# Performance work log

Hardware: AMD Instinct MI355X
Metric: run time of the kernel (lower is better)

## Reference

```python
import jax, jax.numpy as jnp
import numpy as np
from jax.scipy.special import logsumexp


def setup_inputs() -> dict:
    key = jax.random.key(0)
    k = jax.random.split(key, 8)
    B, T, K, L = 32, 128, 16, 16
    s = 0.05
    y_batch = jax.random.uniform(k[0], (B, T, 1, 28, 28), dtype=jnp.float32)
    enc_w1 = jax.random.normal(k[1], (400, 784), dtype=jnp.float32) * s
    enc_b1 = jnp.zeros((400,), jnp.float32)
    enc_w2 = jax.random.normal(k[2], (2 * L, 400), dtype=jnp.float32) * s
    enc_b2 = jnp.zeros((2 * L,), jnp.float32)
    dec_fc_w = jax.random.normal(k[3], (400, L + K), dtype=jnp.float32) * s
    dec_fc_b = jnp.zeros((400,), jnp.float32)
    dec_w = jax.random.normal(k[4], (784, 400), dtype=jnp.float32) * s
    dec_b = jnp.zeros((784,), jnp.float32)
    log_pi = jnp.zeros((K,), jnp.float32)
    log_A = jax.random.normal(k[5], (K, K), dtype=jnp.float32)
    log_A = log_A.at[jnp.arange(K), jnp.arange(K)].set(-1e9)  # fill_diagonal_(-1e9)
    eps = jax.random.normal(k[6], (B * T, L), dtype=jnp.float32)
    return dict(y_batch=y_batch, enc_w1=enc_w1, enc_b1=enc_b1, enc_w2=enc_w2,
                enc_b2=enc_b2, dec_fc_w=dec_fc_w, dec_fc_b=dec_fc_b, dec_w=dec_w,
                dec_b=dec_b, log_pi=log_pi, log_A=log_A, eps=eps)


def reference(y_batch, enc_w1, enc_b1, enc_w2, enc_b2, dec_fc_w, dec_fc_b,
              dec_w, dec_b, log_pi, log_A, eps):
    B, T = y_batch.shape[0], y_batch.shape[1]
    K = log_pi.shape[0]
    L = eps.shape[1]
    N = B * T
    # ---- VAE emission log-likelihoods (compute_log_bk); dropout in eval mode ----
    y_flat = y_batch.reshape(N, 784)
    h = jax.nn.relu(y_flat @ enc_w1.T + enc_b1)                 # [N,400]
    ml = h @ enc_w2.T + enc_b2                                   # [N,2L]
    mu, logvar = ml[:, :L], ml[:, L:]
    z = mu + eps * jnp.exp(0.5 * logvar)                         # reparameterize
    # decode(z, one_hot(k)) for all k at once: split cat-linear into z part + k column
    Wz, Wx = dec_fc_w[:, :L], dec_fc_w[:, L:]                    # [400,L],[400,K]
    base = z @ Wz.T + dec_fc_b                                   # [N,400]
    hk = jax.nn.relu(base[None, :, :] + Wx.T[:, None, :])        # [K,N,400]
    y_rec = jax.nn.sigmoid(jnp.einsum('knh,oh->kno', hk, dec_w) + dec_b)  # [K,N,784]
    # binary_cross_entropy with torch's log clamp at -100
    logp = jnp.clip(jnp.log(y_rec), -100.0, None)
    log1mp = jnp.clip(jnp.log(1.0 - y_rec), -100.0, None)
    bce = -(y_flat[None] * logp + (1.0 - y_flat[None]) * log1mp)  # [K,N,784]
    recon = bce.sum(-1) / 100.0                                   # [K,N]
    log_bk = (-recon).reshape(K, B, T).transpose(1, 2, 0)         # [B,T,K]
    # ---- forward-backward in log domain ----
    lp = jnp.log(jax.nn.softmax(log_pi) + 1e-9)
    lA = jnp.log(jax.nn.softmax(log_A, axis=1) + 1e-9)
    lb_rest = jnp.moveaxis(log_bk[:, 1:], 1, 0)                   # [T-1,B,K]
    a0 = lp + log_bk[:, 0]                                        # [B,K]

    def fstep(prev, lb_t):
        cur = logsumexp(prev[:, :, None] + lA[None], axis=1) + lb_t
        return cur, cur

    _, alphas = jax.lax.scan(fstep, a0, lb_rest)
    log_alpha = jnp.concatenate([a0[:, None], jnp.moveaxis(alphas, 0, 1)], axis=1)  # [B,T,K]

    bT = jnp.zeros((B, K), log_bk.dtype)

    def bstep(nxt, lb_t1):
        cur = logsumexp(lA[None] + (lb_t1 + nxt)[:, None, :], axis=2)
        return cur, cur

    _, betas = jax.lax.scan(bstep, bT, lb_rest, reverse=True)     # betas[t] = beta_t, t=0..T-2
    log_beta = jnp.concatenate([jnp.moveaxis(betas, 0, 1), bT[:, None]], axis=1)  # [B,T,K]

    lg = log_alpha + log_beta
    log_gamma = lg - logsumexp(lg, axis=2, keepdims=True)

    lxi = (log_alpha[:, :-1, :, None] + lA[None, None]
           + (log_bk[:, 1:] + log_beta[:, 1:])[:, :, None, :])    # [B,T-1,K,K]
    lxi = lxi - logsumexp(lxi, axis=(2, 3), keepdims=True)
    return jnp.exp(log_gamma), jnp.exp(lxi)
```

## Files before the change

kernel.cpp:

```cpp
#include <hip/hip_runtime.h>
#include <math.h>


typedef _Float16 h8v __attribute__((ext_vector_type(8)));
typedef _Float16 h4v __attribute__((ext_vector_type(4)));
typedef float f16v __attribute__((ext_vector_type(16)));

__device__ __forceinline__ void gll16(const void* g, void* l) {
  __builtin_amdgcn_global_load_lds(
      (const __attribute__((address_space(1))) void*)g,
      (__attribute__((address_space(3))) void*)l, 16, 0, 0);
}

__global__ __launch_bounds__(256)
void k_prep(const float* __restrict__ dw, const float* __restrict__ ew1,
            _Float16* __restrict__ dwh, _Float16* __restrict__ w1h,
            float* __restrict__ lb) {
  int idx = blockIdx.x * 256 + threadIdx.x;
  if (idx < 65536) lb[idx] = 0.f;
  if (idx < 896 * 448) {
    int o = idx / 448, h2 = idx - o * 448;
    float v = (o < 784 && h2 < 400) ? dw[o * 400 + h2] : 0.f;
    dwh[idx] = (_Float16)v;
  } else if (idx < 896 * 448 + 512 * 800) {
    int j = idx - 896 * 448;
    int i = j / 800, kc = j - i * 800;
    float v = (i < 400 && kc < 784) ? ew1[i * 784 + kc] : 0.f;
    w1h[j] = (_Float16)v;
  }
}

#define E1ST 40
__global__ __launch_bounds__(256, 2)
void k_enc1(const float* __restrict__ y, const _Float16* __restrict__ w1h,
            const float* __restrict__ b1, float* __restrict__ hout) {
  __shared__ __align__(16) _Float16 Ah[64 * E1ST];
  __shared__ __align__(16) _Float16 Bh[128 * E1ST];
  const int tid = threadIdx.x;
  const int i0 = blockIdx.x * 128;
  const int n0 = blockIdx.y * 64;
  const int wav = tid >> 6, lane = tid & 63;
  const int wn = wav >> 1, wi = wav & 1;
  const int ln = lane & 31, kg = lane >> 5;

  f16v acc[2];
#pragma unroll
  for (int j = 0; j < 2; ++j)
#pragma unroll
    for (int r = 0; r < 16; ++r) acc[j][r] = 0.f;

  const int ar = tid >> 3, ac4 = (tid & 7) * 4;
  const int br = tid >> 2, bg = (tid & 3) * 8;

#pragma unroll 1
  for (int hc = 0; hc < 25; ++hc) {
    const int h0 = hc * 32;
    __syncthreads();
#pragma unroll
    for (int it = 0; it < 2; ++it) {
      int r = ar + 32 * it;
      float4 a = make_float4(0.f, 0.f, 0.f, 0.f);
      if (h0 + ac4 < 784) a = *(const float4*)&y[(n0 + r) * 784 + h0 + ac4];
      h4v hv;
      hv[0] = (_Float16)a.x; hv[1] = (_Float16)a.y;
      hv[2] = (_Float16)a.z; hv[3] = (_Float16)a.w;
      *(h4v*)&Ah[r * E1ST + ac4] = hv;
    }
#pragma unroll
    for (int it = 0; it < 2; ++it) {
      int r = br + 64 * it;
      *(h8v*)&Bh[r * E1ST + bg] = *(const h8v*)&w1h[(i0 + r) * 800 + h0 + bg];
    }
    __syncthreads();
#pragma unroll
    for (int kk = 0; kk < 2; ++kk) {
      const int ko = kk * 16 + kg * 8;
      h8v a  = *(const h8v*)&Ah[(wn * 32 + ln) * E1ST + ko];
      h8v b0 = *(const h8v*)&Bh[(wi * 64 + ln) * E1ST + ko];
      h8v b1 = *(const h8v*)&Bh[(wi * 64 + 32 + ln) * E1ST + ko];
      acc[0] = __builtin_amdgcn_mfma_f32_32x32x16_f16(a, b0, acc[0], 0, 0, 0);
      acc[1] = __builtin_amdgcn_mfma_f32_32x32x16_f16(a, b1, acc[1], 0, 0, 0);
    }
  }
#pragma unroll
  for (int j = 0; j < 2; ++j) {
    const int i = i0 + wi * 64 + j * 32 + ln;
    if (i < 400) {
      const float bias = b1[i];
#pragma unroll
      for (int reg = 0; reg < 16; ++reg) {
        const int row = n0 + wn * 32 + (reg & 3) + 8 * (reg >> 2) + 4 * kg;
        hout[row * 400 + i] = fmaxf(acc[j][reg] + bias, 0.f);
      }
    }
  }
}

__global__ __launch_bounds__(128, 2)
void k_enc2z(const float* __restrict__ h, const float* __restrict__ w2,
             const float* __restrict__ b2, const float* __restrict__ eps,
             float* __restrict__ z) {
  __shared__ __align__(16) float h_lds[16 * 400];
  __shared__ __align__(16) float w2_lds[32 * 404];
  __shared__ float ml_lds[16 * 32];
  const int tid = threadIdx.x;
  const int n0 = blockIdx.x * 16;
  for (int idx = tid; idx < 1600; idx += 128) {
    int r = idx / 100, c = idx - r * 100;
    *(float4*)&h_lds[r * 400 + c * 4] = *(const float4*)&h[(n0 + r) * 400 + c * 4];
  }
  for (int idx = tid; idx < 3200; idx += 128) {
    int r = idx / 100, c = idx - r * 100;
    *(float4*)&w2_lds[r * 404 + c * 4] = *(const float4*)&w2[r * 400 + c * 4];
  }
  __syncthreads();
  const int c_ = tid & 31, n4 = tid >> 5;
  float a0 = 0.f, a1 = 0.f, a2 = 0.f, a3 = 0.f;
  for (int q = 0; q < 100; ++q) {
    float4 wv = *(const float4*)&w2_lds[c_ * 404 + q * 4];
    float4 h0 = *(const float4*)&h_lds[(n4 * 4 + 0) * 400 + q * 4];
    float4 h1 = *(const float4*)&h_lds[(n4 * 4 + 1) * 400 + q * 4];
    float4 h2 = *(const float4*)&h_lds[(n4 * 4 + 2) * 400 + q * 4];
    float4 h3 = *(const float4*)&h_lds[(n4 * 4 + 3) * 400 + q * 4];
    a0 += h0.x * wv.x + h0.y * wv.y + h0.z * wv.z + h0.w * wv.w;
    a1 += h1.x * wv.x + h1.y * wv.y + h1.z * wv.z + h1.w * wv.w;
    a2 += h2.x * wv.x + h2.y * wv.y + h2.z * wv.z + h2.w * wv.w;
    a3 += h3.x * wv.x + h3.y * wv.y + h3.z * wv.z + h3.w * wv.w;
  }
  const float bb = b2[c_];
  ml_lds[(n4 * 4 + 0) * 32 + c_] = a0 + bb;
  ml_lds[(n4 * 4 + 1) * 32 + c_] = a1 + bb;
  ml_lds[(n4 * 4 + 2) * 32 + c_] = a2 + bb;
  ml_lds[(n4 * 4 + 3) * 32 + c_] = a3 + bb;
  __syncthreads();
  for (int t = tid; t < 256; t += 128) {
    int n2 = t >> 4, l = t & 15;
    float mu = ml_lds[n2 * 32 + l];
    float lv = ml_lds[n2 * 32 + 16 + l];
    z[(n0 + n2) * 16 + l] = mu + eps[(n0 + n2) * 16 + l] * expf(0.5f * lv);
  }
}

__global__ __launch_bounds__(256, 2)
void k_basehk(const float* __restrict__ z, const float* __restrict__ dfw,
              const float* __restrict__ dfb, _Float16* __restrict__ hkh) {
  __shared__ float z_lds[16 * 16];
  __shared__ __align__(16) float wz[400 * 20];
  __shared__ __align__(16) float base[16 * 448];
  const int tid = threadIdx.x;
  const int n0 = blockIdx.x * 16;
  if (tid < 64) {
    int n = tid >> 2, c = (tid & 3) * 4;
    *(float4*)&z_lds[n * 16 + c] = *(const float4*)&z[(n0 + n) * 16 + c];
  }
  for (int idx = tid; idx < 1600; idx += 256) {
    int i = idx >> 2, c = (idx & 3) * 4;
    *(float4*)&wz[i * 20 + c] = *(const float4*)&dfw[i * 32 + c];
  }
  __syncthreads();
  for (int idx = tid; idx < 7168; idx += 256) {
    int n = idx / 448, i = idx - n * 448;
    float acc = 0.f;
    if (i < 400) {
      acc = dfb[i];
#pragma unroll
      for (int q = 0; q < 4; ++q) {
        float4 zv = *(const float4*)&z_lds[n * 16 + q * 4];
        float4 wv = *(const float4*)&wz[i * 20 + q * 4];
        acc += zv.x * wv.x + zv.y * wv.y + zv.z * wv.z + zv.w * wv.w;
      }
    }
    base[n * 448 + i] = acc;
  }
  __syncthreads();
  for (int idx = tid; idx < 7168; idx += 256) {
    int k = idx / 448, hh = idx - k * 448;
    wz[idx] = (hh < 400) ? dfw[hh * 32 + 16 + k] : 0.f;
  }
  __syncthreads();
  for (int s = tid; s < 14336; s += 256) {
    int k = s / 896, r2 = s - k * 896;
    int r = r2 / 56, c8 = r2 - r * 56;
    const float* bp = &base[r * 448 + c8 * 8];
    const float* wp = &wz[k * 448 + c8 * 8];
    float4 b0 = *(const float4*)bp, b1 = *(const float4*)(bp + 4);
    float4 w0 = *(const float4*)wp, w1 = *(const float4*)(wp + 4);
    h8v o;
    o[0] = (_Float16)fmaxf(b0.x + w0.x, 0.f);
    o[1] = (_Float16)fmaxf(b0.y + w0.y, 0.f);
    o[2] = (_Float16)fmaxf(b0.z + w0.z, 0.f);
    o[3] = (_Float16)fmaxf(b0.w + w0.w, 0.f);
    o[4] = (_Float16)fmaxf(b1.x + w1.x, 0.f);
    o[5] = (_Float16)fmaxf(b1.y + w1.y, 0.f);
    o[6] = (_Float16)fmaxf(b1.z + w1.z, 0.f);
    o[7] = (_Float16)fmaxf(b1.w + w1.w, 0.f);
    *(h8v*)&hkh[((size_t)k * 4096 + n0 + r) * 448 + c8 * 8] = o;
  }
}

__global__ __launch_bounds__(256, 4)
void k_base(const float* __restrict__ z, const float* __restrict__ dfw,
            const float* __restrict__ dfb, float* __restrict__ basep) {
  __shared__ float z_lds[16 * 16];
  __shared__ __align__(16) float wz_lds[400 * 20];
  const int tid = threadIdx.x;
  const int n0 = blockIdx.x * 16;
  if (tid < 64) {
    int n = tid >> 2, c = (tid & 3) * 4;
    *(float4*)&z_lds[n * 16 + c] = *(const float4*)&z[(n0 + n) * 16 + c];
  }
  for (int idx = tid; idx < 1600; idx += 256) {
    int i = idx >> 2, c = (idx & 3) * 4;
    *(float4*)&wz_lds[i * 20 + c] = *(const float4*)&dfw[i * 32 + c];
  }
  __syncthreads();
  for (int idx = tid; idx < 7168; idx += 256) {
    int n = idx / 448, i = idx - n * 448;
    float acc = 0.f;
    if (i < 400) {
      acc = dfb[i];
#pragma unroll
      for (int q = 0; q < 4; ++q) {
        float4 zv = *(const float4*)&z_lds[n * 16 + q * 4];
        float4 wv = *(const float4*)&wz_lds[i * 20 + q * 4];
        acc += zv.x * wv.x + zv.y * wv.y + zv.z * wv.z + zv.w * wv.w;
      }
    }
    basep[(n0 + n) * 448 + i] = acc;
  }
}

__global__ __launch_bounds__(256, 2)
void k_dec5(const _Float16* __restrict__ hkh, const _Float16* __restrict__ dwh,
            const float* __restrict__ decb, const float* __restrict__ y,
            float* __restrict__ lb) {
  __shared__ __align__(16) _Float16 Ah[2][128 * 64];
  __shared__ __align__(16) _Float16 Bh[2][128 * 64];
  __shared__ float red[256];

  const int tid = threadIdx.x;
  const int id  = blockIdx.x;
  const int lin = (id & 7) * 448 + (id >> 3);
  const int n_i = lin / 112;
  const int rem = lin - n_i * 112;
  const int k   = rem / 7;
  const int ot  = rem - k * 7;
  const int n0  = n_i * 128;
  const int o0  = ot * 128;

  const int wav = tid >> 6, lane = tid & 63;
  const int wn = wav >> 1, wo = wav & 1;
  const int ln = lane & 31, kg = lane >> 5;

  const int l8 = lane >> 3, l7 = lane & 7;
  const int swh = (l7 * 8) ^ (l8 * 8);
  const _Float16* hkk = hkh + (size_t)k * (4096 * 448);
  const _Float16* pA[4];
  const _Float16* pB[4];
#pragma unroll
  for (int i = 0; i < 4; ++i) {
    const int row = wav * 32 + i * 8 + l8;
    pA[i] = hkk + (size_t)(n0 + row) * 448 + swh;
    pB[i] = dwh + (size_t)(o0 + row) * 448 + swh;
  }

  f16v acc[2][2];
#pragma unroll
  for (int i = 0; i < 2; ++i)
#pragma unroll
    for (int j = 0; j < 2; ++j)
#pragma unroll
      for (int r = 0; r < 16; ++r) acc[i][j][r] = 0.f;

#pragma unroll
  for (int i = 0; i < 4; ++i) { gll16(pA[i], &Ah[0][(wav * 4 + i) * 512]); pA[i] += 64; }
#pragma unroll
  for (int i = 0; i < 4; ++i) { gll16(pB[i], &Bh[0][(wav * 4 + i) * 512]); pB[i] += 64; }
  asm volatile("s_waitcnt vmcnt(0)" ::: "memory");
  __builtin_amdgcn_sched_barrier(0);
  __builtin_amdgcn_s_barrier();

  const int e0 = (kg * 8) ^ ((ln & 7) * 8);
  const int arow = (wn * 64 + ln) * 64;
  const int brow = (wo * 64 + ln) * 64;

  int cur = 0;
#pragma unroll 1
  for (int hc = 0; hc < 7; ++hc) {
    if (hc < 6) {
#pragma unroll
      for (int i = 0; i < 4; ++i) { gll16(pA[i], &Ah[cur ^ 1][(wav * 4 + i) * 512]); pA[i] += 64; }
#pragma unroll
      for (int i = 0; i < 4; ++i) { gll16(pB[i], &Bh[cur ^ 1][(wav * 4 + i) * 512]); pB[i] += 64; }
      __builtin_amdgcn_sched_barrier(0);
    }
    const _Float16* Ac = Ah[cur];
    const _Float16* Bc = Bh[cur];
#pragma unroll
    for (int kk = 0; kk < 4; ++kk) {
      const int cx = (kk * 16) ^ e0;
      h8v a0 = *(const h8v*)&Ac[arow + cx];
      h8v a1 = *(const h8v*)&Ac[arow + 2048 + cx];
      h8v b0 = *(const h8v*)&Bc[brow + cx];
      h8v b1 = *(const h8v*)&Bc[brow + 2048 + cx];
      acc[0][0] = __builtin_amdgcn_mfma_f32_32x32x16_f16(a0, b0, acc[0][0], 0, 0, 0);
      acc[1][0] = __builtin_amdgcn_mfma_f32_32x32x16_f16(a1, b0, acc[1][0], 0, 0, 0);
      acc[0][1] = __builtin_amdgcn_mfma_f32_32x32x16_f16(a0, b1, acc[0][1], 0, 0, 0);
      acc[1][1] = __builtin_amdgcn_mfma_f32_32x32x16_f16(a1, b1, acc[1][1], 0, 0, 0);
    }
    if (hc < 6) {
      asm volatile("s_waitcnt vmcnt(0)" ::: "memory");
      __builtin_amdgcn_sched_barrier(0);
      __builtin_amdgcn_s_barrier();
      cur ^= 1;
    }
  }

  const int obase = o0 + wo * 64;
  const float bj0 = (obase + ln < 784) ? decb[obase + ln] : 0.f;
  const float bj1 = (obase + 32 + ln < 784) ? decb[obase + 32 + ln] : 0.f;
#pragma unroll
  for (int i = 0; i < 2; ++i) {
#pragma unroll
    for (int reg = 0; reg < 16; ++reg) {
      const int row = wn * 64 + i * 32 + (reg & 3) + 8 * (reg >> 2) + 4 * kg;
      float v = 0.f;
#pragma unroll
      for (int j = 0; j < 2; ++j) {
        const int o = obase + j * 32 + ln;
        if (o < 784) {
          float x = acc[i][j][reg] + (j ? bj1 : bj0);
          float yv = y[(n0 + row) * 784 + o];
          float spx = fmaxf(x, 0.f) + __logf(1.f + __expf(-fabsf(x)));
          v += spx - yv * x;
        }
      }
      v += __shfl_xor(v, 1, 64);
      v += __shfl_xor(v, 2, 64);
      v += __shfl_xor(v, 4, 64);
      v += __shfl_xor(v, 8, 64);
      v += __shfl_xor(v, 16, 64);
      if (ln == 0) red[wo * 128 + row] = v;
    }
  }
  __syncthreads();
  if (tid < 128) {
    float s = red[tid] + red[128 + tid];
    atomicAdd(&lb[(n0 + tid) * 16 + k], s);
  }
}

#define DST 72
__global__ __launch_bounds__(256, 2)
void k_dec1(const float* __restrict__ basep, const float* __restrict__ dfw,
            const _Float16* __restrict__ dwh, const float* __restrict__ decb,
            const float* __restrict__ y, float* __restrict__ lb) {
  __shared__ __align__(16) _Float16 Ah[128 * DST];
  __shared__ __align__(16) _Float16 Bh[128 * DST];
  __shared__ float wx[448];
  __shared__ float red[256];

  const int tid = threadIdx.x;
  const int id  = blockIdx.x;
  const int lin = (id & 7) * 448 + (id >> 3);
  const int n_i = lin / 112;
  const int rem = lin - n_i * 112;
  const int k   = rem / 7;
  const int ot  = rem - k * 7;
  const int n0  = n_i * 128;
  const int o0  = ot * 128;
  const bool full = (ot < 6);

  const int wav = tid >> 6, lane = tid & 63;
  const int wn = wav >> 1, wo = wav & 1;
  const int ln = lane & 31, kg = lane >> 5;

  for (int i = tid; i < 448; i += 256) wx[i] = (i < 400) ? dfw[i * 32 + 16 + k] : 0.f;

  const int ar = tid >> 4, ac4 = (tid & 15) * 4;
  const int br = tid >> 3, bg = (tid & 7) * 8;
  const float* aptr = basep + (long)(n0 + ar) * 448 + ac4;

  float4 apf[8];
#pragma unroll
  for (int it = 0; it < 8; ++it) apf[it] = *(const float4*)&aptr[(16 * it) * 448];

  f16v acc[2][2];
#pragma unroll
  for (int i = 0; i < 2; ++i)
#pragma unroll
    for (int j = 0; j < 2; ++j)
#pragma unroll
      for (int r = 0; r < 16; ++r) acc[i][j][r] = 0.f;

#pragma unroll 1
  for (int hc = 0; hc < 7; ++hc) {
    const int h0 = hc * 64;
    h8v bpf[4];
#pragma unroll
    for (int it = 0; it < 4; ++it)
      bpf[it] = *(const h8v*)&dwh[(o0 + br + 32 * it) * 448 + h0 + bg];
    __syncthreads();
    {
      float4 w = *(const float4*)&wx[h0 + ac4];
#pragma unroll
      for (int it = 0; it < 8; ++it) {
        int r = ar + 16 * it;
        h4v hv;
        hv[0] = (_Float16)fmaxf(apf[it].x + w.x, 0.f);
        hv[1] = (_Float16)fmaxf(apf[it].y + w.y, 0.f);
        hv[2] = (_Float16)fmaxf(apf[it].z + w.z, 0.f);
        hv[3] = (_Float16)fmaxf(apf[it].w + w.w, 0.f);
        *(h4v*)&Ah[r * DST + ac4] = hv;
      }
    }
#pragma unroll
    for (int it = 0; it < 4; ++it)
      *(h8v*)&Bh[(br + 32 * it) * DST + bg] = bpf[it];
    __syncthreads();
    if (hc < 6) {
      const int hn = (hc + 1) * 64;
#pragma unroll
      for (int it = 0; it < 8; ++it)
        apf[it] = *(const float4*)&aptr[(16 * it) * 448 + hn];
    }
#pragma unroll
    for (int kk = 0; kk < 4; ++kk) {
      const int ko = kk * 16 + kg * 8;
      h8v a0 = *(const h8v*)&Ah[(wn * 64 + ln) * DST + ko];
      h8v a1 = *(const h8v*)&Ah[(wn * 64 + 32 + ln) * DST + ko];
      h8v b0 = *(const h8v*)&Bh[(wo * 64 + ln) * DST + ko];
      h8v b1 = *(const h8v*)&Bh[(wo * 64 + 32 + ln) * DST + ko];
      if (full) {
        acc[0][0] = __builtin_amdgcn_mfma_f32_32x32x16_f16(a0, b0, acc[0][0], 0, 0, 0);
        acc[1][0] = __builtin_amdgcn_mfma_f32_32x32x16_f16(a1, b0, acc[1][0], 0, 0, 0);
        acc[0][1] = __builtin_amdgcn_mfma_f32_32x32x16_f16(a0, b1, acc[0][1], 0, 0, 0);
        acc[1][1] = __builtin_amdgcn_mfma_f32_32x32x16_f16(a1, b1, acc[1][1], 0, 0, 0);
      } else if (wo == 0) {
        acc[0][0] = __builtin_amdgcn_mfma_f32_32x32x16_f16(a0, b0, acc[0][0], 0, 0, 0);
        acc[1][0] = __builtin_amdgcn_mfma_f32_32x32x16_f16(a1, b0, acc[1][0], 0, 0, 0);
      }
    }
  }
  const int obase = o0 + wo * 64;
  const float bj0 = (obase + ln < 784) ? decb[obase + ln] : 0.f;
  const float bj1 = (obase + 32 + ln < 784) ? decb[obase + 32 + ln] : 0.f;
#pragma unroll
  for (int i = 0; i < 2; ++i) {
#pragma unroll
    for (int reg = 0; reg < 16; ++reg) {
      const int row = wn * 64 + i * 32 + (reg & 3) + 8 * (reg >> 2) + 4 * kg;
      float v = 0.f;
#pragma unroll
      for (int j = 0; j < 2; ++j) {
        const int o = obase + j * 32 + ln;
        if (o < 784) {
          float x = acc[i][j][reg] + (j ? bj1 : bj0);
          float yv = y[(n0 + row) * 784 + o];
          float spx = fmaxf(x, 0.f) + __logf(1.f + __expf(-fabsf(x)));
          float t2 = fminf(spx, 100.f);
          float t1 = fminf(spx - x, 100.f);
          v += t2 + yv * (t1 - t2);
        }
      }
      v += __shfl_xor(v, 1, 64);
      v += __shfl_xor(v, 2, 64);
      v += __shfl_xor(v, 4, 64);
      v += __shfl_xor(v, 8, 64);
      v += __shfl_xor(v, 16, 64);
      if (ln == 0) red[wo * 128 + row] = v;
    }
  }
  __syncthreads();
  if (tid < 128) {
    float s = red[tid] + red[128 + tid];
    atomicAdd(&lb[(n0 + tid) * 16 + k], s);
  }
}

__global__ __launch_bounds__(256, 2)
void k_hmm(const float* __restrict__ lb, const float* __restrict__ lpi,
           const float* __restrict__ lA, float* __restrict__ out) {
  __shared__ float btl[128 * 16];
  __shared__ float ah[128 * 16];
  __shared__ float bh[128 * 16];
  __shared__ float braw[128 * 16];
  __shared__ float A_l[16 * 17];
  __shared__ float pi_l[16];
  __shared__ float sinv_l[128];
  const int tid = threadIdx.x;
  const int b = blockIdx.x;

  for (int idx = tid; idx < 512; idx += 256) {
    float4 v = *(const float4*)&lb[b * 2048 + idx * 4];
    v.x *= -0.01f; v.y *= -0.01f; v.z *= -0.01f; v.w *= -0.01f;
    *(float4*)&btl[idx * 4] = v;
  }
  if (tid < 16) {
    const int j = tid;
    float m = -1e30f;
#pragma unroll
    for (int q = 0; q < 16; ++q) m = fmaxf(m, lA[j * 16 + q]);
    float e[16]; float s = 0.f;
#pragma unroll
    for (int q = 0; q < 16; ++q) { e[q] = expf(lA[j * 16 + q] - m); s += e[q]; }
    float inv = 1.f / s;
#pragma unroll
    for (int q = 0; q < 16; ++q) A_l[j * 17 + q] = e[q] * inv + 1e-9f;
  } else if (tid == 16) {
    float m = -1e30f;
#pragma unroll
    for (int q = 0; q < 16; ++q) m = fmaxf(m, lpi[q]);
    float e[16]; float s = 0.f;
#pragma unroll
    for (int q = 0; q < 16; ++q) { e[q] = expf(lpi[q] - m); s += e[q]; }
    float inv = 1.f / s;
#pragma unroll
    for (int q = 0; q < 16; ++q) pi_l[q] = e[q] * inv + 1e-9f;
  }
  __syncthreads();
  if (tid < 128) {
    const int t = tid;
    float v[16]; float m = -1e30f;
#pragma unroll
    for (int q = 0; q < 16; ++q) { v[q] = btl[t * 16 + q]; m = fmaxf(m, v[q]); }
#pragma unroll
    for (int q = 0; q < 16; ++q) btl[t * 16 + q] = expf(v[q] - m);
  }
  __syncthreads();
  const int lane = tid & 63;
  const int kk = lane & 15, grp = lane >> 4;
  if (tid < 64) {
    float v0 = pi_l[kk] * btl[kk];
    float ss0 = v0;
    ss0 += __shfl_xor(ss0, 1, 64); ss0 += __shfl_xor(ss0, 2, 64);
    ss0 += __shfl_xor(ss0, 4, 64); ss0 += __shfl_xor(ss0, 8, 64);
    if (grp == 0) ah[kk] = v0 / ss0;
    for (int t = 1; t < 128; ++t) {
      float acc = 0.f;
#pragma unroll
      for (int jj = 0; jj < 4; ++jj) {
        int j = grp * 4 + jj;
        acc = fmaf(ah[(t - 1) * 16 + j], A_l[j * 17 + kk], acc);
      }
      acc += __shfl_xor(acc, 16, 64);
      acc += __shfl_xor(acc, 32, 64);
      float v = acc * btl[t * 16 + kk];
      float ss = v;
      ss += __shfl_xor(ss, 1, 64); ss += __shfl_xor(ss, 2, 64);
      ss += __shfl_xor(ss, 4, 64); ss += __shfl_xor(ss, 8, 64);
      if (grp == 0) ah[t * 16 + kk] = v / ss;
    }
  } else if (tid < 128) {
    if (grp == 0) bh[127 * 16 + kk] = 1.f;
    for (int t = 126; t >= 0; --t) {
      float acc = 0.f;
#pragma unroll
      for (int q = 0; q < 4; ++q) {
        int k2 = grp * 4 + q;
        acc = fmaf(A_l[kk * 17 + k2], btl[(t + 1) * 16 + k2] * bh[(t + 1) * 16 + k2], acc);
      }
      acc += __shfl_xor(acc, 16, 64);
      acc += __shfl_xor(acc, 32, 64);
      float ss = acc;
      ss += __shfl_xor(ss, 1, 64); ss += __shfl_xor(ss, 2, 64);
      ss += __shfl_xor(ss, 4, 64); ss += __shfl_xor(ss, 8, 64);
      if (grp == 0) { braw[t * 16 + kk] = acc; bh[t * 16 + kk] = acc / ss; }
    }
  }
  __syncthreads();
  if (tid < 128) {
    const int t = tid;
    float g[16]; float s2 = 0.f;
#pragma unroll
    for (int q = 0; q < 16; ++q) { g[q] = ah[t * 16 + q] * bh[t * 16 + q]; s2 += g[q]; }
    float inv = 1.f / s2;
#pragma unroll
    for (int c = 0; c < 4; ++c) {
      float4 o;
      o.x = g[c * 4 + 0] * inv; o.y = g[c * 4 + 1] * inv;
      o.z = g[c * 4 + 2] * inv; o.w = g[c * 4 + 3] * inv;
      *(float4*)&out[(b * 128 + t) * 16 + c * 4] = o;
    }
  } else {
    const int t = tid - 128;
    if (t < 127) {
      float s2 = 0.f;
#pragma unroll
      for (int q = 0; q < 16; ++q) s2 += ah[t * 16 + q] * braw[t * 16 + q];
      sinv_l[t] = 1.f / s2;
    }
  }
  __syncthreads();
  const int j = tid >> 4, k2 = tid & 15;
  const float aj = A_l[j * 17 + k2];
  float* xo = out + 65536 + (size_t)b * 127 * 256 + tid;
  for (int t = 0; t < 127; ++t) {
    float val = ah[t * 16 + j] * aj * btl[(t + 1) * 16 + k2] *
                bh[(t + 1) * 16 + k2] * sinv_l[t];
    xo[t * 256] = val;
  }
}

extern "C" void kernel_launch(void* const* d_in, const int* in_sizes, int n_in,
                              void* d_out, int out_size, void* d_ws, size_t ws_size,
                              hipStream_t stream) {
  (void)in_sizes; (void)n_in; (void)out_size;
  const float* y   = (const float*)d_in[0];
  const float* ew1 = (const float*)d_in[1];
  const float* eb1 = (const float*)d_in[2];
  const float* ew2 = (const float*)d_in[3];
  const float* eb2 = (const float*)d_in[4];
  const float* dfw = (const float*)d_in[5];
  const float* dfb = (const float*)d_in[6];
  const float* dw  = (const float*)d_in[7];
  const float* db  = (const float*)d_in[8];
  const float* lpi = (const float*)d_in[9];
  const float* lA  = (const float*)d_in[10];
  const float* eps = (const float*)d_in[11];
  float* out = (float*)d_out;

  float* ws = (float*)d_ws;
  float* h      = ws;
  float* basep  = ws;
  float* z      = ws + 1835008;
  float* lb     = z + 65536;
  _Float16* dwh = (_Float16*)(lb + 65536);
  _Float16* w1h = dwh + 896 * 448;
  float* gpad   = (float*)(w1h + 512 * 800);
  _Float16* hkh = (_Float16*)(gpad + 65536 * 2 + 4096 + 256);

  const bool big_ws = (ws_size >= 68748288ull);

  k_prep<<<3168, 256, 0, stream>>>(dw, ew1, dwh, w1h, lb);
  k_enc1<<<dim3(4, 64), 256, 0, stream>>>(y, w1h, eb1, h);
  k_enc2z<<<256, 128, 0, stream>>>(h, ew2, eb2, eps, z);
  if (big_ws) {
    k_basehk<<<256, 256, 0, stream>>>(z, dfw, dfb, hkh);
    k_dec5<<<3584, 256, 0, stream>>>(hkh, dwh, db, y, lb);
  } else {
    k_base<<<256, 256, 0, stream>>>(z, dfw, dfb, basep);
    k_dec1<<<3584, 256, 0, stream>>>(basep, dfw, dwh, db, y, lb);
  }
  k_hmm<<<32, 256, 0, stream>>>(lb, lpi, lA, out);
}
```

Before: 375.2 us.

## Pre-convert input images to fp16 and single-buffer decoder GEMM LDS tiles

The prep kernel now also converts the input images to a padded fp16 buffer, stored in the hk workspace region before that region is reused. The encoder GEMM then loads 16-byte fp16 vectors instead of converting fp32 on the fly. The decoder GEMM drops its LDS double buffering and uses a single buffer with two barriers per chunk, which halves LDS use and may raise occupancy but exposes load latency. A separate fp32-input encoder remains for the small-workspace path.

Measured after the change: 325.6 us. 1.15x faster.

```diff
diff --git a/kernel.cpp b/kernel.cpp
--- a/kernel.cpp
+++ b/kernel.cpp
@@ -14,7 +14,8 @@
 
 __global__ __launch_bounds__(256)
 void k_prep(const float* __restrict__ dw, const float* __restrict__ ew1,
-            _Float16* __restrict__ dwh, _Float16* __restrict__ w1h,
+            const float* __restrict__ y, _Float16* __restrict__ dwh,
+            _Float16* __restrict__ w1h, _Float16* __restrict__ yh,
             float* __restrict__ lb) {
   int idx = blockIdx.x * 256 + threadIdx.x;
   if (idx < 65536) lb[idx] = 0.f;
@@ -22,18 +23,79 @@
     int o = idx / 448, h2 = idx - o * 448;
     float v = (o < 784 && h2 < 400) ? dw[o * 400 + h2] : 0.f;
     dwh[idx] = (_Float16)v;
-  } else if (idx < 896 * 448 + 512 * 800) {
+  } else if (idx < 811008) {
     int j = idx - 896 * 448;
     int i = j / 800, kc = j - i * 800;
     float v = (i < 400 && kc < 784) ? ew1[i * 784 + kc] : 0.f;
     w1h[j] = (_Float16)v;
+  } else if (idx < 4087808) {
+    int j = idx - 811008;
+    int n = j / 800, c = j - n * 800;
+    float v = (c < 784) ? y[n * 784 + c] : 0.f;
+    yh[j] = (_Float16)v;
   }
 }
 
 #define E1ST 40
 __global__ __launch_bounds__(256, 2)
-void k_enc1(const float* __restrict__ y, const _Float16* __restrict__ w1h,
+void k_enc1(const _Float16* __restrict__ yh, const _Float16* __restrict__ w1h,
             const float* __restrict__ b1, float* __restrict__ hout) {
+  __shared__ __align__(16) _Float16 Ah[64 * E1ST];
+  __shared__ __align__(16) _Float16 Bh[128 * E1ST];
+  const int tid = threadIdx.x;
+  const int i0 = blockIdx.x * 128;
+  const int n0 = blockIdx.y * 64;
+  const int wav = tid >> 6, lane = tid & 63;
+  const int wn = wav >> 1, wi = wav & 1;
+  const int ln = lane & 31, kg = lane >> 5;
+
+  f16v acc[2];
+#pragma unroll
+  for (int j = 0; j < 2; ++j)
+#pragma unroll
+    for (int r = 0; r < 16; ++r) acc[j][r] = 0.f;
+
+  const int ar = tid >> 2, ac8 = (tid & 3) * 8;
+  const int br = tid >> 2, bg = (tid & 3) * 8;
+
+#pragma unroll 1
+  for (int hc = 0; hc < 25; ++hc) {
+    const int h0 = hc * 32;
+    __syncthreads();
+    *(h8v*)&Ah[ar * E1ST + ac8] = *(const h8v*)&yh[(n0 + ar) * 800 + h0 + ac8];
+#pragma unroll
+    for (int it = 0; it < 2; ++it) {
+      int r = br + 64 * it;
+      *(h8v*)&Bh[r * E1ST + bg] = *(const h8v*)&w1h[(i0 + r) * 800 + h0 + bg];
+    }
+    __syncthreads();
+#pragma unroll
+    for (int kk = 0; kk < 2; ++kk) {
+      const int ko = kk * 16 + kg * 8;
+      h8v a  = *(const h8v*)&Ah[(wn * 32 + ln) * E1ST + ko];
+      h8v b0 = *(const h8v*)&Bh[(wi * 64 + ln) * E1ST + ko];
+      h8v b1 = *(const h8v*)&Bh[(wi * 64 + 32 + ln) * E1ST + ko];
+      acc[0] = __builtin_amdgcn_mfma_f32_32x32x16_f16(a, b0, acc[0], 0, 0, 0);
+      acc[1] = __builtin_amdgcn_mfma_f32_32x32x16_f16(a, b1, acc[1], 0, 0, 0);
+    }
+  }
+#pragma unroll
+  for (int j = 0; j < 2; ++j) {
+    const int i = i0 + wi * 64 + j * 32 + ln;
+    if (i < 400) {
+      const float bias = b1[i];
+#pragma unroll
+      for (int reg = 0; reg < 16; ++reg) {
+        const int row = n0 + wn * 32 + (reg & 3) + 8 * (reg >> 2) + 4 * kg;
+        hout[row * 400 + i] = fmaxf(acc[j][reg] + bias, 0.f);
+      }
+    }
+  }
+}
+
+__global__ __launch_bounds__(256, 2)
+void k_enc1f(const float* __restrict__ y, const _Float16* __restrict__ w1h,
+             const float* __restrict__ b1, float* __restrict__ hout) {
   __shared__ __align__(16) _Float16 Ah[64 * E1ST];
   __shared__ __align__(16) _Float16 Bh[128 * E1ST];
   const int tid = threadIdx.x;
@@ -231,11 +293,11 @@
 }
 
 __global__ __launch_bounds__(256, 2)
-void k_dec5(const _Float16* __restrict__ hkh, const _Float16* __restrict__ dwh,
+void k_dec2(const _Float16* __restrict__ hkh, const _Float16* __restrict__ dwh,
             const float* __restrict__ decb, const float* __restrict__ y,
             float* __restrict__ lb) {
-  __shared__ __align__(16) _Float16 Ah[2][128 * 64];
-  __shared__ __align__(16) _Float16 Bh[2][128 * 64];
+  __shared__ __align__(16) _Float16 Ah[128 * 64];
+  __shared__ __align__(16) _Float16 Bh[128 * 64];
   __shared__ float red[256];
 
   const int tid = threadIdx.x;
@@ -272,50 +334,34 @@
 #pragma unroll
       for (int r = 0; r < 16; ++r) acc[i][j][r] = 0.f;
 
-#pragma unroll
-  for (int i = 0; i < 4; ++i) { gll16(pA[i], &Ah[0][(wav * 4 + i) * 512]); pA[i] += 64; }
-#pragma unroll
-  for (int i = 0; i < 4; ++i) { gll16(pB[i], &Bh[0][(wav * 4 + i) * 512]); pB[i] += 64; }
-  asm volatile("s_waitcnt vmcnt(0)" ::: "memory");
-  __builtin_amdgcn_sched_barrier(0);
-  __builtin_amdgcn_s_barrier();
-
-  const int e0 = (kg * 8) ^ ((ln & 7) * 8);
+  const int sx = (ln & 7) * 8;
+  const int e0 = (kg * 8) ^ sx;
   const int arow = (wn * 64 + ln) * 64;
   const int brow = (wo * 64 + ln) * 64;
 
-  int cur = 0;
 #pragma unroll 1
   for (int hc = 0; hc < 7; ++hc) {
-    if (hc < 6) {
-#pragma unroll
-      for (int i = 0; i < 4; ++i) { gll16(pA[i], &Ah[cur ^ 1][(wav * 4 + i) * 512]); pA[i] += 64; }
-#pragma unroll
-      for (int i = 0; i < 4; ++i) { gll16(pB[i], &Bh[cur ^ 1][(wav * 4 + i) * 512]); pB[i] += 64; }
-      __builtin_amdgcn_sched_barrier(0);
-    }
-    const _Float16* Ac = Ah[cur];
-    const _Float16* Bc = Bh[cur];
+    __syncthreads();
+#pragma unroll
+    for (int i = 0; i < 4; ++i) {
+      gll16(pA[i], &Ah[(wav * 4 + i) * 512]);
+      gll16(pB[i], &Bh[(wav * 4 + i) * 512]);
+      pA[i] += 64; pB[i] += 64;
+    }
+    __syncthreads();
 #pragma unroll
     for (int kk = 0; kk < 4; ++kk) {
       const int cx = (kk * 16) ^ e0;
-      h8v a0 = *(const h8v*)&Ac[arow + cx];
-      h8v a1 = *(const h8v*)&Ac[arow + 2048 + cx];
-      h8v b0 = *(const h8v*)&Bc[brow + cx];
-      h8v b1 = *(const h8v*)&Bc[brow + 2048 + cx];
+      h8v a0 = *(const h8v*)&Ah[arow + cx];
+      h8v a1 = *(const h8v*)&Ah[arow + 2048 + cx];
+      h8v b0 = *(const h8v*)&Bh[brow + cx];
+      h8v b1 = *(const h8v*)&Bh[brow + 2048 + cx];
       acc[0][0] = __builtin_amdgcn_mfma_f32_32x32x16_f16(a0, b0, acc[0][0], 0, 0, 0);
       acc[1][0] = __builtin_amdgcn_mfma_f32_32x32x16_f16(a1, b0, acc[1][0], 0, 0, 0);
       acc[0][1] = __builtin_amdgcn_mfma_f32_32x32x16_f16(a0, b1, acc[0][1], 0, 0, 0);
       acc[1][1] = __builtin_amdgcn_mfma_f32_32x32x16_f16(a1, b1, acc[1][1], 0, 0, 0);
     }
-    if (hc < 6) {
-      asm volatile("s_waitcnt vmcnt(0)" ::: "memory");
-      __builtin_amdgcn_sched_barrier(0);
-      __builtin_amdgcn_s_barrier();
-      cur ^= 1;
-    }
-  }
-
+  }
   const int obase = o0 + wo * 64;
   const float bj0 = (obase + ln < 784) ? decb[obase + ln] : 0.f;
   const float bj1 = (obase + 32 + ln < 784) ? decb[obase + 32 + ln] : 0.f;
@@ -629,16 +675,20 @@
   _Float16* w1h = dwh + 896 * 448;
   float* gpad   = (float*)(w1h + 512 * 800);
   _Float16* hkh = (_Float16*)(gpad + 65536 * 2 + 4096 + 256);
+  _Float16* yh  = hkh;
 
   const bool big_ws = (ws_size >= 68748288ull);
 
-  k_prep<<<3168, 256, 0, stream>>>(dw, ew1, dwh, w1h, lb);
-  k_enc1<<<dim3(4, 64), 256, 0, stream>>>(y, w1h, eb1, h);
-  k_enc2z<<<256, 128, 0, stream>>>(h, ew2, eb2, eps, z);
   if (big_ws) {
+    k_prep<<<15968, 256, 0, stream>>>(dw, ew1, y, dwh, w1h, yh, lb);
+    k_enc1<<<dim3(4, 64), 256, 0, stream>>>(yh, w1h, eb1, h);
+    k_enc2z<<<256, 128, 0, stream>>>(h, ew2, eb2, eps, z);
     k_basehk<<<256, 256, 0, stream>>>(z, dfw, dfb, hkh);
-    k_dec5<<<3584, 256, 0, stream>>>(hkh, dwh, db, y, lb);
+    k_dec2<<<3584, 256, 0, stream>>>(hkh, dwh, db, y, lb);
   } else {
+    k_prep<<<3168, 256, 0, stream>>>(dw, ew1, y, dwh, w1h, yh, lb);
+    k_enc1f<<<dim3(4, 64), 256, 0, stream>>>(y, w1h, eb1, h);
+    k_enc2z<<<256, 128, 0, stream>>>(h, ew2, eb2, eps, z);
     k_base<<<256, 256, 0, stream>>>(z, dfw, dfb, basep);
     k_dec1<<<3584, 256, 0, stream>>>(basep, dfw, dwh, db, y, lb);
   }
```
